# Kernel tuning notes

Hardware: AMD Instinct MI355X
Metric: run time of the kernel (lower is better)

The kernel has to match this reference:

```python
import jax, jax.numpy as jnp
import numpy as np
import math

N = 4096
E = 131072
IN_DIM, HID, OUT = 512, 256, 64
DEPTH = 3
RATIO = 0.5


def setup_inputs() -> dict:
    key = jax.random.key(0)
    ks = jax.random.split(key, 12)

    def w(k, fi, fo):
        return jax.random.normal(k, (fi, fo), jnp.float32) * (1.0 / np.sqrt(fi).astype(np.float32))

    return {
        "x": jax.random.normal(ks[0], (N, IN_DIM), jnp.float32),
        "edge_index": jax.random.randint(ks[1], (2, E), 0, N, jnp.int32),
        "dW0": w(ks[2], IN_DIM, HID), "dW1": w(ks[3], HID, HID),
        "dW2": w(ks[4], HID, HID), "dW3": w(ks[5], HID, HID),
        "db0": jnp.zeros((HID,), jnp.float32), "db1": jnp.zeros((HID,), jnp.float32),
        "db2": jnp.zeros((HID,), jnp.float32), "db3": jnp.zeros((HID,), jnp.float32),
        "pw0": jax.random.normal(ks[6], (HID,), jnp.float32),
        "pw1": jax.random.normal(ks[7], (HID,), jnp.float32),
        "pw2": jax.random.normal(ks[8], (HID,), jnp.float32),
        "uW0": w(ks[9], HID, HID), "uW1": w(ks[10], HID, HID), "uW2": w(ks[11], HID, OUT),
        "ub0": jnp.zeros((HID,), jnp.float32), "ub1": jnp.zeros((HID,), jnp.float32),
        "ub2": jnp.zeros((OUT,), jnp.float32),
    }


def gcn_conv(x, A, W, b):
    # GCNConv(improved=True): A_hat = A + 2I, sym-normalized.
    n = A.shape[0]
    eye = jnp.eye(n, dtype=A.dtype)
    Ah = A + 2.0 * eye
    d = Ah.sum(axis=1)
    dinv = jnp.where(d > 0, jax.lax.rsqrt(d), 0.0)
    An = dinv[:, None] * Ah * dinv[None, :]
    return An @ (x @ W) + b


def augment_adj(A):
    # add self loops, square the (weighted) adjacency, remove self loops
    n = A.shape[0]
    eye = jnp.eye(n, dtype=A.dtype)
    Al = A + eye
    A2 = Al @ Al
    return A2 * (1.0 - eye)


def topk_pool(x, A, w, k):
    # TopKPooling: score = tanh(x.w/||w||); keep top-k; gate kept features by score.
    score = jnp.tanh((x @ w) / jnp.linalg.norm(w))
    _, perm = jax.lax.top_k(score, k)
    xp = x[perm] * score[perm][:, None]
    return xp, A[perm][:, perm], perm


def _forward(x, edge_index, down_Ws, down_bs, pool_ws, up_Ws, up_bs):
    A = jnp.zeros((N, N), jnp.float32).at[edge_index[0], edge_index[1]].set(1.0)
    x = jax.nn.relu(gcn_conv(x, A, down_Ws[0], down_bs[0]))
    xs, As, perms = [x], [A], []
    n = N
    for i in range(1, DEPTH + 1):
        A = augment_adj(A)
        k = int(math.ceil(RATIO * n)); n = k
        x, A, perm = topk_pool(x, A, pool_ws[i - 1], k)
        x = jax.nn.relu(gcn_conv(x, A, down_Ws[i], down_bs[i]))
        if i < DEPTH:
            xs.append(x); As.append(A)
        perms.append(perm)
    for i in range(DEPTH):
        j = DEPTH - 1 - i
        res, A, perm = xs[j], As[j], perms[j]
        up = jnp.zeros_like(res).at[perm].set(x)   # unpool (sum_res=True)
        x = res + up
        x = gcn_conv(x, A, up_Ws[i], up_bs[i])
        if i < DEPTH - 1:
            x = jax.nn.relu(x)
    return x


def reference(x, edge_index, dW0, dW1, dW2, dW3, db0, db1, db2, db3,
              pw0, pw1, pw2, uW0, uW1, uW2, ub0, ub1, ub2):
    return _forward(x, edge_index,
                    [dW0, dW1, dW2, dW3], [db0, db1, db2, db3],
                    [pw0, pw1, pw2],
                    [uW0, uW1, uW2], [ub0, ub1, ub2])
```

## Files before the change

### kernel.cpp

```cpp
#include <hip/hip_runtime.h>
#include <math.h>

#define NN 4096
#define EE 131072
#define IN_DIM 512
#define HID 256
#define OUT_DIM 64
#define ECAP 128

typedef __attribute__((ext_vector_type(8))) short bf8_t;
typedef __attribute__((ext_vector_type(4))) float f4_t;
typedef __attribute__((ext_vector_type(8))) unsigned short us8_t;
typedef __attribute__((ext_vector_type(4))) unsigned short us4_t;

#define GAS __attribute__((address_space(1)))
#define LAS __attribute__((address_space(3)))

__device__ __forceinline__ unsigned short f2bf(float v){
  union { float f; unsigned u; } x; x.f = v;
  unsigned r = x.u + 0x7fffu + ((x.u >> 16) & 1u);
  return (unsigned short)(r >> 16);
}
__device__ __forceinline__ float bf2f(unsigned short h){
  union { float f; unsigned u; } x; x.u = ((unsigned)h) << 16;
  return x.f;
}

__device__ __forceinline__ float waveReduceSum(float v){
#pragma unroll
  for (int off = 32; off > 0; off >>= 1) v += __shfl_down(v, off);
  return v;
}

__global__ __launch_bounds__(256) void k_prep(
    const float* __restrict__ x_in, const float* __restrict__ dW0,
    const float* __restrict__ dW1, const float* __restrict__ dW2,
    const float* __restrict__ dW3, const float* __restrict__ uW0,
    const float* __restrict__ uW1, const float* __restrict__ uW2,
    unsigned* __restrict__ bits,
    unsigned short* __restrict__ xinh, unsigned short* __restrict__ xinl,
    unsigned short* __restrict__ W0th, unsigned short* __restrict__ W0tl,
    unsigned short* __restrict__ W5th, unsigned short* __restrict__ W5tl,
    unsigned short* __restrict__ W2th, unsigned short* __restrict__ W2tl)
{
  int b = blockIdx.x;
  if (b < 128){
    int base = b * 4096 + threadIdx.x;
#pragma unroll
    for (int i = 0; i < 16; ++i) bits[base + i * 256] = 0;
    return;
  }
  b -= 128;
  if (b < 2048){
    int i0 = b * 1024 + threadIdx.x;
#pragma unroll
    for (int i = 0; i < 4; ++i){
      int idx = i0 + i * 256;
      float v = x_in[idx];
      unsigned short h = f2bf(v);
      xinh[idx] = h; xinl[idx] = f2bf(v - bf2f(h));
    }
    return;
  }
  b -= 2048;
  const float* X; unsigned short *Th, *Tl; int R, C, tile;
  if (b < 128){ X = dW0; Th = W0th; Tl = W0tl; R = 512; C = 256; tile = b; }
  else if (b < 448){
    int t2 = b - 128; int z = t2 >> 6; int rem = t2 & 63;
    const float* ws[5] = {dW1, dW2, dW3, uW0, uW1};
    X = ws[z]; Th = W5th + (size_t)z * 65536; Tl = W5tl + (size_t)z * 65536;
    R = 256; C = 256; tile = rem;
  } else { X = uW2; Th = W2th; Tl = W2tl; R = 256; C = 64; tile = b - 448; }
  int tpr = C >> 5;
  int bx = (tile % tpr) * 32, by = (tile / tpr) * 32;
  __shared__ float t[32][33];
  int tx = threadIdx.x & 31, ty = threadIdx.x >> 5;
#pragma unroll
  for (int i = 0; i < 4; ++i)
    t[ty + i * 8][tx] = X[(size_t)(by + ty + i * 8) * C + bx + tx];
  __syncthreads();
#pragma unroll
  for (int i = 0; i < 4; ++i){
    float v = t[tx][ty + i * 8];
    unsigned short h = f2bf(v);
    size_t o = (size_t)(bx + ty + i * 8) * R + by + tx;
    Th[o] = h; Tl[o] = f2bf(v - bf2f(h));
  }
}

__global__ void k_build_bits(const int* __restrict__ ei, unsigned* __restrict__ bits){
  int e = blockIdx.x * blockDim.x + threadIdx.x;
  if (e < EE){
    int r = ei[e], c = ei[EE + e];
    atomicOr(&bits[r * 128 + (c >> 5)], 1u << (c & 31));
  }
}

__global__ __launch_bounds__(128) void k_ell(const unsigned* __restrict__ bits,
                                             int* __restrict__ ell, int* __restrict__ cnt,
                                             float* __restrict__ dinv){
  int r = blockIdx.x, t = threadIdx.x;
  unsigned w = bits[r * 128 + t];
  int c = __popc(w);
  __shared__ int sc[128];
  sc[t] = c; __syncthreads();
  for (int off = 1; off < 128; off <<= 1){
    int a = sc[t], b = (t >= off) ? sc[t - off] : 0;
    __syncthreads(); sc[t] = a + b; __syncthreads();
  }
  int total = sc[127];
  int pos = sc[t] - c;
  int base = r * ECAP;
  while (w){
    int b = __ffs(w) - 1; w &= w - 1;
    if (pos < ECAP) ell[base + pos] = t * 32 + b;
    pos++;
  }
  if (t == 0){
    cnt[r] = (total < ECAP) ? total : ECAP;
    dinv[r] = 1.0f / sqrtf((float)total + 2.0f);
  }
}

template<int NCOLS, int RELU, int SC>
__global__ __launch_bounds__(256) void k_spmm_ell(
    const int* __restrict__ ell, const int* __restrict__ cnt,
    const float* __restrict__ Zs, const float* __restrict__ dinv,
    const float* __restrict__ bias, float* __restrict__ out,
    const float* __restrict__ scw, float* __restrict__ score)
{
  int r = blockIdx.x;
  __shared__ int s_idx[ECAP];
  __shared__ int s_n;
  __shared__ float sh[4 * NCOLS];
  __shared__ float sd[4], sq[4];
  if (threadIdx.x == 0) s_n = cnt[r];
  for (int i = threadIdx.x; i < ECAP; i += 256) s_idx[i] = ell[r * ECAP + i];
  __syncthreads();
  int n = s_n; if (n > ECAP) n = ECAP;
  int wv = threadIdx.x >> 6, lane = threadIdx.x & 63;
  if (NCOLS == 256){
    f4_t acc = (f4_t){0.f, 0.f, 0.f, 0.f};
    for (int e = wv; e < n; e += 4){
      const f4_t* row = (const f4_t*)(Zs + (size_t)s_idx[e] * 256);
      acc += row[lane];
    }
    ((f4_t*)(sh + wv * 256))[lane] = acc;
  } else {
    float acc = 0.f;
    for (int e = wv; e < n; e += 4)
      acc += Zs[(size_t)s_idx[e] * 64 + lane];
    sh[wv * 64 + lane] = acc;
  }
  __syncthreads();
  int t = threadIdx.x;
  float o = 0.f;
  if (t < NCOLS){
    float y = sh[t] + sh[NCOLS + t] + sh[2 * NCOLS + t] + sh[3 * NCOLS + t];
    float z = Zs[(size_t)r * NCOLS + t];
    o = dinv[r] * (y + 2.0f * z) + bias[t];
    if (RELU) o = fmaxf(o, 0.f);
    out[(size_t)r * NCOLS + t] = o;
  }
  if (SC){
    float w = scw[t];
    float d = waveReduceSum(o * w);
    float q = waveReduceSum(w * w);
    if (!lane){ sd[wv] = d; sq[wv] = q; }
    __syncthreads();
    if (!t) score[r] = tanhf((sd[0] + sd[1] + sd[2] + sd[3]) / sqrtf(sq[0] + sq[1] + sq[2] + sq[3]));
  }
}

__global__ __launch_bounds__(256) void k_pool_build(
    const float* __restrict__ x0, const float* __restrict__ score,
    const int* __restrict__ perm1, const int* __restrict__ inv1,
    const int* __restrict__ ell, const int* __restrict__ cnt,
    unsigned short* __restrict__ xph, unsigned short* __restrict__ xpl,
    unsigned short* __restrict__ Rb2,
    unsigned short* __restrict__ xu1h, unsigned short* __restrict__ xu1l)
{
  int b = blockIdx.x;
  if (b < 2048){
    int pr = perm1[b]; float s = score[pr];
    int c = threadIdx.x;
    float v = x0[(size_t)pr * 256 + c] * s;
    unsigned short h = f2bf(v);
    xph[(size_t)b * 256 + c] = h;
    xpl[(size_t)b * 256 + c] = f2bf(v - bf2f(h));
    return;
  }
  if (b < 6144){
    int k = b - 2048;
    __shared__ unsigned char row[2048];
    for (int i = threadIdx.x; i < 512; i += 256) ((int*)row)[i] = 0;
    __syncthreads();
    int n = cnt[k];
    for (int e = threadIdx.x; e < n; e += 256){
      int s = inv1[ell[k * ECAP + e]];
      if (s >= 0) row[s] = 1;
    }
    __syncthreads();
    if (threadIdx.x == 0){
      int sk = inv1[k];
      if (sk >= 0) row[sk] += 1;
    }
    __syncthreads();
    unsigned w = 0;
#pragma unroll
    for (int j = 0; j < 8; ++j) w |= ((unsigned)row[(threadIdx.x << 3) + j]) << (2 * j);
    Rb2[k * 256 + threadIdx.x] = (unsigned short)w;
    return;
  }
  int r = b - 6144;
  if (inv1[r] < 0){
    int c = threadIdx.x;
    float v = x0[(size_t)r * 256 + c];
    unsigned short h = f2bf(v);
    xu1h[(size_t)r * 256 + c] = h;
    xu1l[(size_t)r * 256 + c] = f2bf(v - bf2f(h));
  }
}

template<int SRCL, int OUTL>
__global__ __launch_bounds__(256) void k_pp(
    const float* __restrict__ x, const float* __restrict__ score,
    const int* __restrict__ perm, const int* __restrict__ inv, int n, int k,
    unsigned short* __restrict__ xph, unsigned short* __restrict__ xpl,
    unsigned short* __restrict__ xuh, unsigned short* __restrict__ xul,
    const unsigned short* __restrict__ Ah, const unsigned short* __restrict__ Al,
    unsigned short* __restrict__ Lh, unsigned short* __restrict__ Ll,
    unsigned short* __restrict__ Rh, unsigned short* __restrict__ Rl)
{
  __shared__ float t[32][33];
  __shared__ int sinv[32];
  int b = blockIdx.x, c = threadIdx.x;
  if (b < k){
    int pr = perm[b]; float s = score[pr];
    float v = x[(size_t)pr * 256 + c] * s;
    unsigned short h = f2bf(v);
    xph[(size_t)b * 256 + c] = h;
    xpl[(size_t)b * 256 + c] = f2bf(v - bf2f(h));
    return;
  }
  b -= k;
  if (b < n){
    if (inv[b] < 0){
      float v = x[(size_t)b * 256 + c];
      unsigned short h = f2bf(v);
      xuh[(size_t)b * 256 + c] = h;
      xul[(size_t)b * 256 + c] = f2bf(v - bf2f(h));
    }
    return;
  }
  b -= n;
  if (b < k){
    int r = b, pr = perm[r];
    for (int cc = threadIdx.x; cc < n; cc += 256){
      float v = bf2f(Ah[(size_t)pr * n + cc]);
      if (SRCL) v += bf2f(Al[(size_t)pr * n + cc]);
      if (pr == cc) v += 1.f;
      unsigned short h = f2bf(v);
      Lh[(size_t)r * n + cc] = h;
      if (OUTL) Ll[(size_t)r * n + cc] = f2bf(v - bf2f(h));
    }
    return;
  }
  b -= k;
  int tpr = n >> 5;
  int kt = b / tpr, ct = b - kt * tpr;
  int tx = threadIdx.x & 31, ty = threadIdx.x >> 5;
  if (threadIdx.x < 32) sinv[threadIdx.x] = inv[ct * 32 + threadIdx.x];
#pragma unroll
  for (int i = 0; i < 4; ++i){
    int kl = ty + i * 8;
    size_t src = (size_t)(kt * 32 + kl) * n + ct * 32 + tx;
    float v = bf2f(Ah[src]);
    if (SRCL) v += bf2f(Al[src]);
    t[kl][tx] = v;
  }
  __syncthreads();
#pragma unroll
  for (int i = 0; i < 4; ++i){
    int cl = ty + i * 8;
    int s = sinv[cl];
    if (s >= 0){
      float v = t[tx][cl];
      if (kt * 32 + tx == ct * 32 + cl) v += 1.f;
      unsigned short h = f2bf(v);
      size_t o = (size_t)s * n + kt * 32 + tx;
      Rh[o] = h;
      if (OUTL) Rl[o] = f2bf(v - bf2f(h));
    }
  }
}

__global__ __launch_bounds__(256) void k_sq1(const int* __restrict__ ell, const int* __restrict__ cnt,
                                             const int* __restrict__ perm,
                                             const unsigned short* __restrict__ Rb2,
                                             unsigned short* __restrict__ A1h,
                                             float* __restrict__ dinv1){
  int r = blockIdx.x;
  int pr = perm[r];
  __shared__ int s_idx[ECAP];
  __shared__ int s_n;
  __shared__ float sred[4];
  if (threadIdx.x == 0) s_n = cnt[pr];
  for (int i = threadIdx.x; i < ECAP; i += 256) s_idx[i] = ell[pr * ECAP + i];
  __syncthreads();
  int n = s_n; if (n > ECAP) n = ECAP;
  int colb = threadIdx.x * 8;
  auto expand = [](unsigned x) -> uint2 {
    uint2 e;
    e.x = (x & 3) | (((x >> 2) & 3) << 8) | (((x >> 4) & 3) << 16) | (((x >> 6) & 3) << 24);
    e.y = ((x >> 8) & 3) | (((x >> 10) & 3) << 8) | (((x >> 12) & 3) << 16) | (((x >> 14) & 3) << 24);
    return e;
  };
  uint2 acc = expand(Rb2[pr * 256 + threadIdx.x]);
  for (int e = 0; e < n; ++e){
    uint2 v = expand(Rb2[s_idx[e] * 256 + threadIdx.x]);
    acc.x += v.x; acc.y += v.y;
  }
  float fs = 0.f;
  us8_t o;
#pragma unroll
  for (int j = 0; j < 8; ++j){
    unsigned byte = ((j < 4 ? acc.x : acc.y) >> (8 * (j & 3))) & 0xFFu;
    if (colb + j == r) byte = 0;
    float f = (float)byte;
    fs += f;
    o[j] = f2bf(f);
  }
  *(us8_t*)(A1h + (size_t)r * 2048 + colb) = o;
  fs = waveReduceSum(fs);
  int lane = threadIdx.x & 63, wd = threadIdx.x >> 6;
  if (!lane) sred[wd] = fs;
  __syncthreads();
  if (!threadIdx.x)
    dinv1[r] = 1.0f / sqrtf(sred[0] + sred[1] + sred[2] + sred[3] + 2.0f);
}

template<int HAS_AL, int HAS_BL, int HAS_LL, int EPI>
__global__ __launch_bounds__(256) void k_mm(
    const unsigned short* __restrict__ Ah, const unsigned short* __restrict__ Al,
    const unsigned short* __restrict__ Bh, const unsigned short* __restrict__ Bl,
    int M, int N, int K, int KS, float* __restrict__ P,
    float* __restrict__ Cf, unsigned short* __restrict__ Ch, unsigned short* __restrict__ Cl,
    const float* __restrict__ dinv)
{
  constexpr int NARR = 2 + HAS_AL + HAS_BL;
  constexpr int BUF = NARR * 8192;
  __shared__ int4 ldsq[NARR * 512 * 2];
  char* ldsc = (char*)ldsq;

  const int tid = threadIdx.x, lane = tid & 63, wid = tid >> 6;
  const int wm = wid >> 1, wn = wid & 1;
  const int nbx = gridDim.x, nby = gridDim.y;
  const int tot = nbx * nby * gridDim.z;
  int id = blockIdx.x + nbx * (blockIdx.y + nby * blockIdx.z);
  if ((tot & 7) == 0) id = (id & 7) * (tot >> 3) + (id >> 3);
  const int sx = id % nbx; int remq = id / nbx;
  const int sy = remq % nby;
  const int bm = sy << 6, bn = sx << 6;
  const int z = remq / nby;
  const int l15 = lane & 15, l4 = lane >> 4;

  f4_t acc[2][2];
#pragma unroll
  for (int i = 0; i < 2; ++i)
#pragma unroll
    for (int j = 0; j < 2; ++j) acc[i][j] = (f4_t){0.f, 0.f, 0.f, 0.f};

  const size_t rb = (size_t)K * 2;
  const size_t kz = (size_t)z * KS * 2;
  const char* pAh = (const char*)Ah + (size_t)bm * rb;
  const char* pAl = HAS_AL ? (const char*)Al + (size_t)bm * rb : nullptr;
  const char* pBh = (const char*)Bh + (size_t)bn * rb;
  const char* pBl = HAS_BL ? (const char*)Bl + (size_t)bn * rb : nullptr;

  auto stage = [&](int t, int b2){
    char* ldsb = ldsc + b2 * BUF;
    const size_t kb = kz + (size_t)t * 128;
#pragma unroll
    for (int it = 0; it < 2; ++it){
      const int idx = tid + (it << 8);
      const int row = idx >> 3;
      const int kc = ((idx & 7) << 4) ^ ((row & 7) << 4);
      const size_t go = (size_t)row * rb + kb + kc;
      const int lo = idx * 16;
      __builtin_amdgcn_global_load_lds((const GAS void*)(pAh + go), (LAS void*)(ldsb + lo), 16, 0, 0);
      __builtin_amdgcn_global_load_lds((const GAS void*)(pBh + go), (LAS void*)(ldsb + 8192 + lo), 16, 0, 0);
      if (HAS_AL)
        __builtin_amdgcn_global_load_lds((const GAS void*)(pAl + go), (LAS void*)(ldsb + 16384 + lo), 16, 0, 0);
      if (HAS_BL)
        __builtin_amdgcn_global_load_lds((const GAS void*)(pBl + go), (LAS void*)(ldsb + (2 + HAS_AL) * 8192 + lo), 16, 0, 0);
    }
  };

  const int T = KS >> 6;
  stage(0, 0);
  int b = 0;
  for (int t = 0; t < T; ++t){
    if (t + 1 < T){
      stage(t + 1, b ^ 1);
      if constexpr (NARR == 2) asm volatile("s_waitcnt vmcnt(4)" ::: "memory");
      else if constexpr (NARR == 3) asm volatile("s_waitcnt vmcnt(6)" ::: "memory");
      else asm volatile("s_waitcnt vmcnt(8)" ::: "memory");
    } else {
      asm volatile("s_waitcnt vmcnt(0)" ::: "memory");
    }
    __syncthreads();
    const char* ldsb = ldsc + b * BUF;
#pragma unroll
    for (int ks = 0; ks < 2; ++ks){
      bf8_t aH[2], aL[2], bH[2], bL[2];
#pragma unroll
      for (int f = 0; f < 2; ++f){
        int ar = wm * 32 + f * 16 + l15;
        int aoff = ar * 128 + (((ks * 64) + (l4 << 4)) ^ ((ar & 7) << 4));
        aH[f] = *(const bf8_t*)(ldsb + aoff);
        if (HAS_AL) aL[f] = *(const bf8_t*)(ldsb + 16384 + aoff);
        int br = wn * 32 + f * 16 + l15;
        int boff = br * 128 + (((ks * 64) + (l4 << 4)) ^ ((br & 7) << 4));
        bH[f] = *(const bf8_t*)(ldsb + 8192 + boff);
        if (HAS_BL) bL[f] = *(const bf8_t*)(ldsb + (2 + HAS_AL) * 8192 + boff);
      }
#pragma unroll
      for (int i = 0; i < 2; ++i)
#pragma unroll
        for (int j = 0; j < 2; ++j){
          acc[i][j] = __builtin_amdgcn_mfma_f32_16x16x32_bf16(aH[i], bH[j], acc[i][j], 0, 0, 0);
          if (HAS_BL) acc[i][j] = __builtin_amdgcn_mfma_f32_16x16x32_bf16(aH[i], bL[j], acc[i][j], 0, 0, 0);
          if (HAS_AL) acc[i][j] = __builtin_amdgcn_mfma_f32_16x16x32_bf16(aL[i], bH[j], acc[i][j], 0, 0, 0);
          if (HAS_LL) acc[i][j] = __builtin_amdgcn_mfma_f32_16x16x32_bf16(aL[i], bL[j], acc[i][j], 0, 0, 0);
        }
    }
    __syncthreads();
    b ^= 1;
  }

  float* Pz = (EPI == 0) ? P + (size_t)z * M * N : nullptr;
#pragma unroll
  for (int i = 0; i < 2; ++i)
#pragma unroll
    for (int j = 0; j < 2; ++j)
#pragma unroll
      for (int r = 0; r < 4; ++r){
        int grow = bm + wm * 32 + i * 16 + l4 * 4 + r;
        int gcol = bn + wn * 32 + j * 16 + l15;
        float v = acc[i][j][r];
        size_t o = (size_t)grow * N + gcol;
        if (EPI == 0){
          Pz[o] = v;
        } else if (EPI == 2){
          Cf[o] = dinv[grow] * v;
        } else {
          float sv = dinv[grow] * v;
          Cf[o] = sv;
          unsigned short h = f2bf(sv);
          size_t ot = (size_t)gcol * M + grow;
          Ch[ot] = h; Cl[ot] = f2bf(sv - bf2f(h));
        }
      }
}

template<int EPI, int SC, int Z>
__global__ __launch_bounds__(256) void k_red(
    const float* __restrict__ P, int M, int NC,
    const float* __restrict__ dinv, const float* __restrict__ Zs,
    const float* __restrict__ bias,
    float* __restrict__ Of, unsigned short* __restrict__ Oh, unsigned short* __restrict__ Ol,
    float* __restrict__ dout, int relu,
    const float* __restrict__ scw, float* __restrict__ score,
    const float* __restrict__ res, const int* __restrict__ permsel)
{
  int w = threadIdx.x >> 6, lane = threadIdx.x & 63;
  int row = blockIdx.x * 4 + w;
  int prow = (EPI == 4) ? permsel[row] : 0;
  float di = (EPI != 3) ? dinv[row] : 0.f;
  float rsum = 0.f, o_d = 0.f, o_q = 0.f;
  for (int c0 = lane * 4; c0 < NC; c0 += 256){
    size_t o = (size_t)row * NC + c0;
    f4_t s = *(const f4_t*)(P + o);
#pragma unroll
    for (int zz = 1; zz < Z; ++zz) s += *(const f4_t*)(P + (size_t)zz * M * NC + o);
    if (EPI == 2){
      f4_t z4 = *(const f4_t*)(Zs + o);
      f4_t b4 = *(const f4_t*)(bias + c0);
      f4_t out;
#pragma unroll
      for (int j = 0; j < 4; ++j){
        float v = di * (s[j] + 2.0f * z4[j]) + b4[j];
        if (relu) v = fmaxf(v, 0.f);
        out[j] = v;
      }
      *(f4_t*)(Of + o) = out;
      if (SC){
        f4_t w4 = *(const f4_t*)(scw + c0);
#pragma unroll
        for (int j = 0; j < 4; ++j){ o_d += out[j] * w4[j]; o_q += w4[j] * w4[j]; }
      }
    } else if (EPI == 3){
      us4_t h4, l4v;
#pragma unroll
      for (int j = 0; j < 4; ++j){
        float v = (c0 + j == row) ? 0.f : s[j];
        unsigned short h = f2bf(v);
        h4[j] = h; l4v[j] = f2bf(v - bf2f(h));
        rsum += v;
      }
      *(us4_t*)(Oh + o) = h4;
      *(us4_t*)(Ol + o) = l4v;
    } else {
      f4_t z4 = *(const f4_t*)(Zs + o);
      f4_t b4 = *(const f4_t*)(bias + c0);
      f4_t r4 = *(const f4_t*)(res + (size_t)prow * NC + c0);
      us4_t h4, l4v;
#pragma unroll
      for (int j = 0; j < 4; ++j){
        float v = di * (s[j] + 2.0f * z4[j]) + b4[j];
        if (relu) v = fmaxf(v, 0.f);
        float comb = r4[j] + v;
        unsigned short h = f2bf(comb);
        h4[j] = h; l4v[j] = f2bf(comb - bf2f(h));
      }
      size_t od = (size_t)prow * NC + c0;
      *(us4_t*)(Oh + od) = h4;
      *(us4_t*)(Ol + od) = l4v;
    }
  }
  if (EPI == 3){
    rsum = waveReduceSum(rsum);
    if (!lane) dout[row] = 1.0f / sqrtf(rsum + 2.0f);
  }
  if (SC){
    o_d = waveReduceSum(o_d);
    o_q = waveReduceSum(o_q);
    if (!lane) score[row] = tanhf(o_d / sqrtf(o_q));
  }
}

__global__ void k_topk(const float* __restrict__ score, int n, int k,
                       int* __restrict__ perm, int* __restrict__ inv){
  int i = blockIdx.x; float si = score[i];
  int cnt = 0;
  for (int j = threadIdx.x; j < n; j += 256){
    float sj = score[j];
    if (sj > si || (sj == si && j < i)) cnt++;
  }
#pragma unroll
  for (int off = 32; off > 0; off >>= 1) cnt += __shfl_down(cnt, off);
  __shared__ int sh[4];
  int lane = threadIdx.x & 63, wid = threadIdx.x >> 6;
  if (lane == 0) sh[wid] = cnt;
  __syncthreads();
  if (threadIdx.x == 0){
    int rank = sh[0] + sh[1] + sh[2] + sh[3];
    if (rank < k){ perm[rank] = i; inv[i] = rank; }
    else inv[i] = -1;
  }
}

extern "C" void kernel_launch(void* const* d_in, const int* in_sizes, int n_in,
                              void* d_out, int out_size, void* d_ws, size_t ws_size,
                              hipStream_t stream){
  (void)in_sizes; (void)n_in; (void)out_size;
  const float* x_in = (const float*)d_in[0];
  const int*   ei   = (const int*)d_in[1];
  const float* dW0 = (const float*)d_in[2];
  const float* dW1 = (const float*)d_in[3];
  const float* dW2 = (const float*)d_in[4];
  const float* dW3 = (const float*)d_in[5];
  const float* db0 = (const float*)d_in[6];
  const float* db1 = (const float*)d_in[7];
  const float* db2 = (const float*)d_in[8];
  const float* db3 = (const float*)d_in[9];
  const float* pw0 = (const float*)d_in[10];
  const float* pw1 = (const float*)d_in[11];
  const float* pw2 = (const float*)d_in[12];
  const float* uW0 = (const float*)d_in[13];
  const float* uW1 = (const float*)d_in[14];
  const float* uW2 = (const float*)d_in[15];
  const float* ub0 = (const float*)d_in[16];
  const float* ub1 = (const float*)d_in[17];
  const float* ub2 = (const float*)d_in[18];

  char* p = (char*)d_ws;
  auto alloc = [&](size_t nbytes) -> void* {
    void* q = (void*)p; p += (nbytes + 255) & ~(size_t)255; return q;
  };
  unsigned* bits = (unsigned*)alloc((size_t)4096 * 128 * 4);
  int* ell = (int*)alloc((size_t)4096 * ECAP * 4);
  int* cnt = (int*)alloc(4096 * 4);
  int* inv1 = (int*)alloc(4096 * 4);
  int* inv2 = (int*)alloc(2048 * 4);
  int* inv3 = (int*)alloc(1024 * 4);
  unsigned short* Rb2 = (unsigned short*)alloc((size_t)4096 * 256 * 2);
  float* Pp = (float*)alloc((size_t)8 * 1024 * 1024);
  unsigned short* A1h = (unsigned short*)alloc((size_t)2048 * 2048 * 2);
  unsigned short* A2h = (unsigned short*)alloc((size_t)1024 * 1024 * 2);
  unsigned short* A2l = (unsigned short*)alloc((size_t)1024 * 1024 * 2);
  unsigned short* A3h = (unsigned short*)alloc((size_t)512 * 512 * 2);
  unsigned short* A3l = (unsigned short*)alloc((size_t)512 * 512 * 2);
  unsigned short* Lb2h = (unsigned short*)alloc((size_t)1024 * 2048 * 2);
  unsigned short* Rt2h = (unsigned short*)alloc((size_t)1024 * 2048 * 2);
  unsigned short* Lb3h = (unsigned short*)alloc((size_t)512 * 1024 * 2);
  unsigned short* Lb3l = (unsigned short*)alloc((size_t)512 * 1024 * 2);
  unsigned short* Rt3h = (unsigned short*)alloc((size_t)512 * 1024 * 2);
  unsigned short* Rt3l = (unsigned short*)alloc((size_t)512 * 1024 * 2);
  unsigned short* xinh = (unsigned short*)alloc((size_t)4096 * 512 * 2);
  unsigned short* xinl = (unsigned short*)alloc((size_t)4096 * 512 * 2);
  float* x0 = (float*)alloc((size_t)4096 * HID * 4);
  float* x1 = (float*)alloc((size_t)2048 * HID * 4);
  float* x2 = (float*)alloc((size_t)1024 * HID * 4);
  unsigned short* xu1h = (unsigned short*)alloc((size_t)4096 * HID * 2);
  unsigned short* xu1l = (unsigned short*)alloc((size_t)4096 * HID * 2);
  unsigned short* xu2h = (unsigned short*)alloc((size_t)2048 * HID * 2);
  unsigned short* xu2l = (unsigned short*)alloc((size_t)2048 * HID * 2);
  unsigned short* xu3h = (unsigned short*)alloc((size_t)1024 * HID * 2);
  unsigned short* xu3l = (unsigned short*)alloc((size_t)1024 * HID * 2);
  unsigned short* xph = (unsigned short*)alloc((size_t)2048 * HID * 2);
  unsigned short* xpl = (unsigned short*)alloc((size_t)2048 * HID * 2);
  unsigned short* W0th = (unsigned short*)alloc((size_t)256 * 512 * 2);
  unsigned short* W0tl = (unsigned short*)alloc((size_t)256 * 512 * 2);
  unsigned short* W5th = (unsigned short*)alloc((size_t)5 * 256 * 256 * 2);
  unsigned short* W5tl = (unsigned short*)alloc((size_t)5 * 256 * 256 * 2);
  unsigned short* W2th = (unsigned short*)alloc((size_t)64 * 256 * 2);
  unsigned short* W2tl = (unsigned short*)alloc((size_t)64 * 256 * 2);
  float* Zs  = (float*)alloc((size_t)4096 * HID * 4);
  unsigned short* ZsTh = (unsigned short*)alloc((size_t)256 * 2048 * 2);
  unsigned short* ZsTl = (unsigned short*)alloc((size_t)256 * 2048 * 2);
  float* dinv0 = (float*)alloc(4096 * 4);
  float* dinv1 = (float*)alloc(2048 * 4);
  float* dinv2 = (float*)alloc(1024 * 4);
  float* dinv3 = (float*)alloc(512 * 4);
  float* score = (float*)alloc(4096 * 4);
  int* perm1 = (int*)alloc(2048 * 4);
  int* perm2 = (int*)alloc(1024 * 4);
  int* perm3 = (int*)alloc(512 * 4);
  if ((size_t)(p - (char*)d_ws) > ws_size) return;

  k_prep<<<2640, 256, 0, stream>>>(x_in, dW0, dW1, dW2, dW3, uW0, uW1, uW2, bits,
                                   xinh, xinl, W0th, W0tl, W5th, W5tl, W2th, W2tl);
  k_build_bits<<<EE / 256, 256, 0, stream>>>(ei, bits);
  k_ell<<<4096, 128, 0, stream>>>(bits, ell, cnt, dinv0);

  { dim3 g(4, 64);
    k_mm<1,1,0,2><<<g, 256, 0, stream>>>(xinh, xinl, W0th, W0tl, 4096, HID, IN_DIM, IN_DIM,
                                         nullptr, Zs, nullptr, nullptr, dinv0); }
  k_spmm_ell<256,1,1><<<4096, 256, 0, stream>>>(ell, cnt, Zs, dinv0, db0, x0, pw0, score);

  k_topk<<<4096, 256, 0, stream>>>(score, 4096, 2048, perm1, inv1);
  k_pool_build<<<10240, 256, 0, stream>>>(x0, score, perm1, inv1, ell, cnt,
                                          xph, xpl, Rb2, xu1h, xu1l);
  k_sq1<<<2048, 256, 0, stream>>>(ell, cnt, perm1, Rb2, A1h, dinv1);
  { dim3 g(4, 32);
    k_mm<1,1,0,4><<<g, 256, 0, stream>>>(xph, xpl, W5th, W5tl, 2048, HID, HID, HID,
                                         nullptr, Zs, ZsTh, ZsTl, dinv1); }
  { dim3 g(4, 32, 4);
    k_mm<0,1,0,0><<<g, 256, 0, stream>>>(A1h, nullptr, ZsTh, ZsTl, 2048, HID, 2048, 512,
                                         Pp, nullptr, nullptr, nullptr, nullptr); }
  k_red<2,1,4><<<512, 256, 0, stream>>>(Pp, 2048, 256, dinv1, Zs, db1,
                                        x1, nullptr, nullptr, nullptr, 1, pw1, score, nullptr, nullptr);

  k_topk<<<2048, 256, 0, stream>>>(score, 2048, 1024, perm2, inv2);
  k_pp<0,0><<<8192, 256, 0, stream>>>(x1, score, perm2, inv2, 2048, 1024,
                                      xph, xpl, xu2h, xu2l, A1h, nullptr,
                                      Lb2h, nullptr, Rt2h, nullptr);
  { dim3 g(16, 16, 2);
    k_mm<0,0,0,0><<<g, 256, 0, stream>>>(Lb2h, nullptr, Rt2h, nullptr, 1024, 1024, 2048, 1024,
                                         Pp, nullptr, nullptr, nullptr, nullptr); }
  k_red<3,0,2><<<256, 256, 0, stream>>>(Pp, 1024, 1024, nullptr, nullptr, nullptr,
                                        nullptr, A2h, A2l, dinv2, 0, nullptr, nullptr, nullptr, nullptr);
  { dim3 g(4, 16);
    k_mm<1,1,0,4><<<g, 256, 0, stream>>>(xph, xpl, W5th + 65536, W5tl + 65536, 1024, HID, HID, HID,
                                         nullptr, Zs, ZsTh, ZsTl, dinv2); }
  { dim3 g(4, 16, 4);
    k_mm<1,1,0,0><<<g, 256, 0, stream>>>(A2h, A2l, ZsTh, ZsTl, 1024, HID, 1024, 256,
                                         Pp, nullptr, nullptr, nullptr, nullptr); }
  k_red<2,1,4><<<256, 256, 0, stream>>>(Pp, 1024, 256, dinv2, Zs, db2,
                                        x2, nullptr, nullptr, nullptr, 1, pw2, score, nullptr, nullptr);

  k_topk<<<1024, 256, 0, stream>>>(score, 1024, 512, perm3, inv3);
  k_pp<1,1><<<3072, 256, 0, stream>>>(x2, score, perm3, inv3, 1024, 512,
                                      xph, xpl, xu3h, xu3l, A2h, A2l,
                                      Lb3h, Lb3l, Rt3h, Rt3l);
  { dim3 g(8, 8, 4);
    k_mm<1,1,1,0><<<g, 256, 0, stream>>>(Lb3h, Lb3l, Rt3h, Rt3l, 512, 512, 1024, 256,
                                         Pp, nullptr, nullptr, nullptr, nullptr); }
  k_red<3,0,4><<<128, 256, 0, stream>>>(Pp, 512, 512, nullptr, nullptr, nullptr,
                                        nullptr, A3h, A3l, dinv3, 0, nullptr, nullptr, nullptr, nullptr);
  { dim3 g(4, 8);
    k_mm<1,1,0,4><<<g, 256, 0, stream>>>(xph, xpl, W5th + 2 * 65536, W5tl + 2 * 65536, 512, HID, HID, HID,
                                         nullptr, Zs, ZsTh, ZsTl, dinv3); }
  { dim3 g(4, 8, 4);
    k_mm<1,1,0,0><<<g, 256, 0, stream>>>(A3h, A3l, ZsTh, ZsTl, 512, HID, 512, 128,
                                         Pp, nullptr, nullptr, nullptr, nullptr); }
  k_red<4,0,4><<<128, 256, 0, stream>>>(Pp, 512, 256, dinv3, Zs, db3,
                                        nullptr, xu3h, xu3l, nullptr, 1, nullptr, nullptr, x2, perm3);

  { dim3 g(4, 16);
    k_mm<1,1,0,4><<<g, 256, 0, stream>>>(xu3h, xu3l, W5th + 3 * 65536, W5tl + 3 * 65536, 1024, HID, HID, HID,
                                         nullptr, Zs, ZsTh, ZsTl, dinv2); }
  { dim3 g(4, 16, 4);
    k_mm<1,1,0,0><<<g, 256, 0, stream>>>(A2h, A2l, ZsTh, ZsTl, 1024, HID, 1024, 256,
                                         Pp, nullptr, nullptr, nullptr, nullptr); }
  k_red<4,0,4><<<256, 256, 0, stream>>>(Pp, 1024, 256, dinv2, Zs, ub0,
                                        nullptr, xu2h, xu2l, nullptr, 1, nullptr, nullptr, x1, perm2);

  { dim3 g(4, 32);
    k_mm<1,1,0,4><<<g, 256, 0, stream>>>(xu2h, xu2l, W5th + 4 * 65536, W5tl + 4 * 65536, 2048, HID, HID, HID,
                                         nullptr, Zs, ZsTh, ZsTl, dinv1); }
  { dim3 g(4, 32, 4);
    k_mm<0,1,0,0><<<g, 256, 0, stream>>>(A1h, nullptr, ZsTh, ZsTl, 2048, HID, 2048, 512,
                                         Pp, nullptr, nullptr, nullptr, nullptr); }
  k_red<4,0,4><<<512, 256, 0, stream>>>(Pp, 2048, 256, dinv1, Zs, ub1,
                                        nullptr, xu1h, xu1l, nullptr, 1, nullptr, nullptr, x0, perm1);

  { dim3 g(1, 64);
    k_mm<1,1,0,2><<<g, 256, 0, stream>>>(xu1h, xu1l, W2th, W2tl, 4096, OUT_DIM, HID, HID,
                                         nullptr, Zs, nullptr, nullptr, dinv0); }
  k_spmm_ell<64,0,0><<<4096, 256, 0, stream>>>(ell, cnt, Zs, dinv0, ub2, (float*)d_out, nullptr, nullptr);
}
```

Baseline: 228.2 us.

## Stage transposed bf16 split epilogue through LDS, deepen split-K, trim ELL loads

The EPI==4 GEMM epilogue used to write the transposed hi/lo bf16 outputs with scattered 2-byte stores. It now stages the scaled tile in LDS and emits coalesced 16-byte vector stores of the transposed data. Separately, the 1024x1024x2048 A2 squaring GEMM goes from split-K 2 to split-K 4, which doubles the partial buffer and the reduction reads in exchange for more blocks. The SpMM kernel now loads only the first cnt ELL indices instead of all 128, at the cost of an extra barrier.

```diff
diff --git a/kernel.cpp b/kernel.cpp
--- a/kernel.cpp
+++ b/kernel.cpp
@@ -135,9 +135,10 @@
   __shared__ float sh[4 * NCOLS];
   __shared__ float sd[4], sq[4];
   if (threadIdx.x == 0) s_n = cnt[r];
-  for (int i = threadIdx.x; i < ECAP; i += 256) s_idx[i] = ell[r * ECAP + i];
   __syncthreads();
   int n = s_n; if (n > ECAP) n = ECAP;
+  for (int i = threadIdx.x; i < n; i += 256) s_idx[i] = ell[r * ECAP + i];
+  __syncthreads();
   int wv = threadIdx.x >> 6, lane = threadIdx.x & 63;
   if (NCOLS == 256){
     f4_t acc = (f4_t){0.f, 0.f, 0.f, 0.f};
@@ -439,6 +440,44 @@
     b ^= 1;
   }
 
+  if (EPI == 4){
+    float* LT = (float*)ldsc;
+#pragma unroll
+    for (int i = 0; i < 2; ++i)
+#pragma unroll
+      for (int j = 0; j < 2; ++j)
+#pragma unroll
+        for (int r = 0; r < 4; ++r){
+          int lr = wm * 32 + i * 16 + l4 * 4 + r;
+          int lc = wn * 32 + j * 16 + l15;
+          float sv = dinv[bm + lr] * acc[i][j][r];
+          Cf[(size_t)(bm + lr) * N + bn + lc] = sv;
+          LT[lr * 68 + lc] = sv;
+        }
+    __syncthreads();
+    int col = tid >> 2;
+    int seg = (tid & 3) << 4;
+    us8_t h0, h1, l0, l1;
+#pragma unroll
+    for (int mm = 0; mm < 8; ++mm){
+      float v = LT[(seg + mm) * 68 + col];
+      unsigned short h = f2bf(v);
+      h0[mm] = h; l0[mm] = f2bf(v - bf2f(h));
+    }
+#pragma unroll
+    for (int mm = 0; mm < 8; ++mm){
+      float v = LT[(seg + 8 + mm) * 68 + col];
+      unsigned short h = f2bf(v);
+      h1[mm] = h; l1[mm] = f2bf(v - bf2f(h));
+    }
+    size_t ob = (size_t)(bn + col) * M + bm + seg;
+    *(us8_t*)(Ch + ob) = h0;
+    *(us8_t*)(Ch + ob + 8) = h1;
+    *(us8_t*)(Cl + ob) = l0;
+    *(us8_t*)(Cl + ob + 8) = l1;
+    return;
+  }
+
   float* Pz = (EPI == 0) ? P + (size_t)z * M * N : nullptr;
 #pragma unroll
   for (int i = 0; i < 2; ++i)
@@ -452,14 +491,8 @@
         size_t o = (size_t)grow * N + gcol;
         if (EPI == 0){
           Pz[o] = v;
-        } else if (EPI == 2){
+        } else {
           Cf[o] = dinv[grow] * v;
-        } else {
-          float sv = dinv[grow] * v;
-          Cf[o] = sv;
-          unsigned short h = f2bf(sv);
-          size_t ot = (size_t)gcol * M + grow;
-          Ch[ot] = h; Cl[ot] = f2bf(sv - bf2f(h));
         }
       }
 }
@@ -596,7 +629,7 @@
   int* inv2 = (int*)alloc(2048 * 4);
   int* inv3 = (int*)alloc(1024 * 4);
   unsigned short* Rb2 = (unsigned short*)alloc((size_t)4096 * 256 * 2);
-  float* Pp = (float*)alloc((size_t)8 * 1024 * 1024);
+  float* Pp = (float*)alloc((size_t)16 * 1024 * 1024);
   unsigned short* A1h = (unsigned short*)alloc((size_t)2048 * 2048 * 2);
   unsigned short* A2h = (unsigned short*)alloc((size_t)1024 * 1024 * 2);
   unsigned short* A2l = (unsigned short*)alloc((size_t)1024 * 1024 * 2);
@@ -667,10 +700,10 @@
   k_pp<0,0><<<8192, 256, 0, stream>>>(x1, score, perm2, inv2, 2048, 1024,
                                       xph, xpl, xu2h, xu2l, A1h, nullptr,
                                       Lb2h, nullptr, Rt2h, nullptr);
-  { dim3 g(16, 16, 2);
-    k_mm<0,0,0,0><<<g, 256, 0, stream>>>(Lb2h, nullptr, Rt2h, nullptr, 1024, 1024, 2048, 1024,
+  { dim3 g(16, 16, 4);
+    k_mm<0,0,0,0><<<g, 256, 0, stream>>>(Lb2h, nullptr, Rt2h, nullptr, 1024, 1024, 2048, 512,
                                          Pp, nullptr, nullptr, nullptr, nullptr); }
-  k_red<3,0,2><<<256, 256, 0, stream>>>(Pp, 1024, 1024, nullptr, nullptr, nullptr,
+  k_red<3,0,4><<<256, 256, 0, stream>>>(Pp, 1024, 1024, nullptr, nullptr, nullptr,
                                         nullptr, A2h, A2l, dinv2, 0, nullptr, nullptr, nullptr, nullptr);
   { dim3 g(4, 16);
     k_mm<1,1,0,4><<<g, 256, 0, stream>>>(xph, xpl, W5th + 65536, W5tl + 65536, 1024, HID, HID, HID,
```

After: 224.9 us. Within noise of the previous version (-1.5%).
